# Optimization experiments

Hardware: AMD Instinct MI355X
Metric: run time of the kernel (lower is better)

Reference implementation:

```python
import jax, jax.numpy as jnp
import numpy as np

EPS = 1e-9


def _squash(s, axis=-1):
    # squash(s) = (|s|^2 / (1+|s|^2)) * s / |s|
    sq = jnp.sum(jnp.square(s), axis=axis, keepdims=True)
    norm = jnp.sqrt(sq + EPS)
    return (sq / (1.0 + sq)) * (s / norm)


def setup_inputs() -> dict:
    key = jax.random.key(0)
    B, N_IN, N_OUT, ATOMS = 32, 2048, 64, 16
    votes = jax.random.normal(key, (B, N_IN, N_OUT, ATOMS), dtype=jnp.float32)
    return {"votes": votes, "num_routing": 3}


def reference(votes, num_routing):
    # votes: [B, in_caps, out_caps, atoms]
    temper = 1.0
    softmax_in = False
    B, n_in, n_out, atoms = votes.shape
    logits = jnp.zeros((B, n_in, n_out, 1), dtype=votes.dtype)
    pose = None
    for i in range(num_routing):
        # coupling coefficients: softmax over out-caps axis (softmax_in=False)
        ax = 1 if softmax_in else 2
        c = jax.nn.softmax(logits * temper, axis=ax)  # [B, in, out, 1]
        # weighted pooling over input capsules -> [B, 1, out, atoms]
        preact = jnp.sum(c * votes, axis=1, keepdims=True)
        pose = _squash(preact, axis=-1)
        if i < num_routing - 1:
            # agreement: <votes, pose> over atoms -> [B, in, out, 1]
            logits = logits + jnp.sum(votes * pose, axis=-1, keepdims=True)
    prob = jnp.sqrt(jnp.sum(jnp.square(pose), axis=-1, keepdims=True) + EPS)  # [B,1,out,1]
    pose_out = jnp.squeeze(pose, axis=-3)          # [B, out, atoms]
    prob_out = jnp.squeeze(prob, axis=(-3, -1))    # [B, out]
    return pose_out, prob_out
```

## Files before the change

kernel.cpp:

```cpp
#include <hip/hip_runtime.h>


#define NB 32
#define NIN 2048
#define NOUT 64
#define ATOMS 16
#define EPSF 1e-9f

#define ROWS_PER_WAVE 8
#define WAVES_PER_BLOCK 4
#define ROWS_PER_BLOCK (ROWS_PER_WAVE * WAVES_PER_BLOCK)
#define CHUNKS (NIN / ROWS_PER_BLOCK)
#define RBATCH 4

template <int USE_POSE>
__global__ __launch_bounds__(256, 4) void route_pass(
    const float* __restrict__ votes,
    const float* __restrict__ pose_accum,
    float* __restrict__ preact)
{
    const int b     = blockIdx.x / CHUNKS;
    const int chunk = blockIdx.x % CHUNKS;
    const int wave  = threadIdx.x >> 6;
    const int lane  = threadIdx.x & 63;

    float pose[ATOMS];
    if (USE_POSE) {
        const float4* p4 = reinterpret_cast<const float4*>(pose_accum) + (b * NOUT + lane) * 4;
        float4 q0 = p4[0], q1 = p4[1], q2 = p4[2], q3 = p4[3];
        pose[0]=q0.x; pose[1]=q0.y; pose[2]=q0.z; pose[3]=q0.w;
        pose[4]=q1.x; pose[5]=q1.y; pose[6]=q1.z; pose[7]=q1.w;
        pose[8]=q2.x; pose[9]=q2.y; pose[10]=q2.z; pose[11]=q2.w;
        pose[12]=q3.x; pose[13]=q3.y; pose[14]=q3.z; pose[15]=q3.w;
    }

    float acc[ATOMS];
#pragma unroll
    for (int a = 0; a < ATOMS; ++a) acc[a] = 0.0f;

    const int in0 = chunk * ROWS_PER_BLOCK + wave * ROWS_PER_WAVE;
    const float4* vrow = reinterpret_cast<const float4*>(votes)
                       + ((size_t)(b * NIN + in0) * NOUT + lane) * (ATOMS / 4);

    for (int r0 = 0; r0 < ROWS_PER_WAVE; r0 += RBATCH) {
        float4 c[RBATCH][4];
#pragma unroll
        for (int r = 0; r < RBATCH; ++r) {
            const float4* vp = vrow + (size_t)(r0 + r) * (NOUT * (ATOMS / 4));
            c[r][0] = vp[0]; c[r][1] = vp[1]; c[r][2] = vp[2]; c[r][3] = vp[3];
        }

        float cc[RBATCH];
        if (USE_POSE) {
            float s[RBATCH], e[RBATCH];
#pragma unroll
            for (int r = 0; r < RBATCH; ++r) {
                const float* v = reinterpret_cast<const float*>(&c[r][0]);
                float logit = 0.0f;
#pragma unroll
                for (int a = 0; a < ATOMS; ++a) logit = fmaf(v[a], pose[a], logit);
                e[r] = __expf(logit);
                s[r] = e[r];
            }
#pragma unroll
            for (int mask = 32; mask >= 1; mask >>= 1) {
#pragma unroll
                for (int r = 0; r < RBATCH; ++r)
                    s[r] += __shfl_xor(s[r], mask, 64);
            }
#pragma unroll
            for (int r = 0; r < RBATCH; ++r) cc[r] = e[r] / s[r];
        } else {
#pragma unroll
            for (int r = 0; r < RBATCH; ++r) cc[r] = 1.0f / 64.0f;
        }
#pragma unroll
        for (int r = 0; r < RBATCH; ++r) {
            const float* v = reinterpret_cast<const float*>(&c[r][0]);
#pragma unroll
            for (int a = 0; a < ATOMS; ++a) acc[a] = fmaf(cc[r], v[a], acc[a]);
        }
    }

    __shared__ float red[WAVES_PER_BLOCK * NOUT * ATOMS];
#pragma unroll
    for (int a = 0; a < ATOMS; ++a)
        red[(wave * NOUT + lane) * ATOMS + a] = acc[a];
    __syncthreads();

    for (int idx = threadIdx.x; idx < NOUT * ATOMS; idx += 256) {
        float t = red[idx] + red[NOUT * ATOMS + idx]
                + red[2 * NOUT * ATOMS + idx] + red[3 * NOUT * ATOMS + idx];
        atomicAdd(&preact[b * NOUT * ATOMS + idx], t);
    }
}

__global__ __launch_bounds__(256) void squash_k(
    const float* __restrict__ preact_in,
    float* __restrict__ preact_clr,
    float* __restrict__ pose_accum,
    float* __restrict__ d_out,
    int mode)
{
    int idx = blockIdx.x * 256 + threadIdx.x;
    float s = preact_in[idx];
    float sq = s * s;
#pragma unroll
    for (int mask = 1; mask < ATOMS; mask <<= 1)
        sq += __shfl_xor(sq, mask, 64);
    float norm = sqrtf(sq + EPSF);
    float f = (sq / (1.0f + sq)) / norm;
    float p = f * s;
    if (mode == 0) {
        pose_accum[idx] = p;
        preact_clr[idx] = 0.0f;
    } else if (mode == 1) {
        pose_accum[idx] += p;
        preact_clr[idx] = 0.0f;
    } else {
        d_out[idx] = p;
        if ((idx & (ATOMS - 1)) == 0) {
            float psq = f * f * sq;
            d_out[NB * NOUT * ATOMS + (idx >> 4)] = sqrtf(psq + EPSF);
        }
    }
}

extern "C" void kernel_launch(void* const* d_in, const int* in_sizes, int n_in,
                              void* d_out, int out_size, void* d_ws, size_t ws_size,
                              hipStream_t stream) {
    const float* votes = (const float*)d_in[0];
    float* out = (float*)d_out;

    float* preact     = (float*)d_ws;
    float* pose_accum = preact + NB * NOUT * ATOMS;
    const size_t pre_bytes = (size_t)NB * NOUT * ATOMS * sizeof(float);

    dim3 blk(256);
    dim3 grid_route(NB * CHUNKS);
    dim3 grid_sq(NB * NOUT * ATOMS / 256);

    hipMemsetAsync(preact, 0, pre_bytes, stream);

    route_pass<0><<<grid_route, blk, 0, stream>>>(votes, nullptr, preact);
    squash_k<<<grid_sq, blk, 0, stream>>>(preact, preact, pose_accum, nullptr, 0);

    route_pass<1><<<grid_route, blk, 0, stream>>>(votes, pose_accum, preact);
    squash_k<<<grid_sq, blk, 0, stream>>>(preact, preact, pose_accum, nullptr, 1);

    route_pass<1><<<grid_route, blk, 0, stream>>>(votes, pose_accum, preact);
    squash_k<<<grid_sq, blk, 0, stream>>>(preact, nullptr, nullptr, out, 2);
}
```

Measured before the change: 458.3 us.

## Cache votes as bf16 in first pass and replace atomics with partial-sum reduction

The first routing pass now also writes a bf16 copy of the votes tensor, and the later passes read that half-size copy instead of the fp32 original. This cuts global memory traffic in the two bandwidth-bound agreement passes. Per-block atomicAdd into preact is replaced by per-chunk partial sums that the squash kernel reduces, which also removes the memset. The cost is an extra bf16 write in pass 0, a larger workspace, and reduced precision in the later routing iterations.

```diff
diff --git a/kernel.cpp b/kernel.cpp
--- a/kernel.cpp
+++ b/kernel.cpp
@@ -13,19 +13,82 @@
 #define CHUNKS (NIN / ROWS_PER_BLOCK)
 #define RBATCH 4
 
-template <int USE_POSE>
-__global__ __launch_bounds__(256, 4) void route_pass(
+__device__ __forceinline__ unsigned pack2_bf16(float lo, float hi) {
+    unsigned ul = __float_as_uint(lo);
+    unsigned uh = __float_as_uint(hi);
+    ul = (ul + 0x7fffu + ((ul >> 16) & 1u)) >> 16;
+    uh = (uh + 0x7fffu + ((uh >> 16) & 1u)) & 0xffff0000u;
+    return ul | uh;
+}
+
+__global__ __launch_bounds__(256, 4) void route_pass0(
     const float* __restrict__ votes,
-    const float* __restrict__ pose_accum,
-    float* __restrict__ preact)
+    uint4* __restrict__ votes_bf16,
+    float* __restrict__ partials)
 {
     const int b     = blockIdx.x / CHUNKS;
     const int chunk = blockIdx.x % CHUNKS;
     const int wave  = threadIdx.x >> 6;
     const int lane  = threadIdx.x & 63;
 
+    float acc[ATOMS];
+#pragma unroll
+    for (int a = 0; a < ATOMS; ++a) acc[a] = 0.0f;
+
+    const int in0 = chunk * ROWS_PER_BLOCK + wave * ROWS_PER_WAVE;
+    const float4* vrow = reinterpret_cast<const float4*>(votes)
+                       + ((size_t)(b * NIN + in0) * NOUT + lane) * 4;
+    uint4* brow = votes_bf16 + ((size_t)(b * NIN + in0) * NOUT + lane) * 2;
+
+    for (int r0 = 0; r0 < ROWS_PER_WAVE; r0 += RBATCH) {
+        float4 c[RBATCH][4];
+#pragma unroll
+        for (int r = 0; r < RBATCH; ++r) {
+            const float4* vp = vrow + (size_t)(r0 + r) * (NOUT * 4);
+            c[r][0] = vp[0]; c[r][1] = vp[1]; c[r][2] = vp[2]; c[r][3] = vp[3];
+        }
+#pragma unroll
+        for (int r = 0; r < RBATCH; ++r) {
+            const float* v = reinterpret_cast<const float*>(&c[r][0]);
+#pragma unroll
+            for (int a = 0; a < ATOMS; ++a) acc[a] += v[a];
+            uint4 p0, p1;
+            p0.x = pack2_bf16(v[0],  v[1]);  p0.y = pack2_bf16(v[2],  v[3]);
+            p0.z = pack2_bf16(v[4],  v[5]);  p0.w = pack2_bf16(v[6],  v[7]);
+            p1.x = pack2_bf16(v[8],  v[9]);  p1.y = pack2_bf16(v[10], v[11]);
+            p1.z = pack2_bf16(v[12], v[13]); p1.w = pack2_bf16(v[14], v[15]);
+            uint4* bp = brow + (size_t)(r0 + r) * (NOUT * 2);
+            bp[0] = p0; bp[1] = p1;
+        }
+    }
+#pragma unroll
+    for (int a = 0; a < ATOMS; ++a) acc[a] *= (1.0f / 64.0f);
+
+    __shared__ float red[WAVES_PER_BLOCK * NOUT * ATOMS];
+#pragma unroll
+    for (int a = 0; a < ATOMS; ++a)
+        red[(wave * NOUT + lane) * ATOMS + a] = acc[a];
+    __syncthreads();
+
+    float* pblock = partials + ((size_t)(b * CHUNKS + chunk) << 10);
+    for (int idx = threadIdx.x; idx < NOUT * ATOMS; idx += 256) {
+        pblock[idx] = red[idx] + red[NOUT * ATOMS + idx]
+                    + red[2 * NOUT * ATOMS + idx] + red[3 * NOUT * ATOMS + idx];
+    }
+}
+
+__global__ __launch_bounds__(256, 4) void route_passN(
+    const uint4* __restrict__ votes_bf16,
+    const float* __restrict__ pose_accum,
+    float* __restrict__ partials)
+{
+    const int b     = blockIdx.x / CHUNKS;
+    const int chunk = blockIdx.x % CHUNKS;
+    const int wave  = threadIdx.x >> 6;
+    const int lane  = threadIdx.x & 63;
+
     float pose[ATOMS];
-    if (USE_POSE) {
+    {
         const float4* p4 = reinterpret_cast<const float4*>(pose_accum) + (b * NOUT + lane) * 4;
         float4 q0 = p4[0], q1 = p4[1], q2 = p4[2], q3 = p4[3];
         pose[0]=q0.x; pose[1]=q0.y; pose[2]=q0.z; pose[3]=q0.w;
@@ -39,46 +102,45 @@
     for (int a = 0; a < ATOMS; ++a) acc[a] = 0.0f;
 
     const int in0 = chunk * ROWS_PER_BLOCK + wave * ROWS_PER_WAVE;
-    const float4* vrow = reinterpret_cast<const float4*>(votes)
-                       + ((size_t)(b * NIN + in0) * NOUT + lane) * (ATOMS / 4);
+    const uint4* brow = votes_bf16 + ((size_t)(b * NIN + in0) * NOUT + lane) * 2;
 
     for (int r0 = 0; r0 < ROWS_PER_WAVE; r0 += RBATCH) {
-        float4 c[RBATCH][4];
-#pragma unroll
-        for (int r = 0; r < RBATCH; ++r) {
-            const float4* vp = vrow + (size_t)(r0 + r) * (NOUT * (ATOMS / 4));
-            c[r][0] = vp[0]; c[r][1] = vp[1]; c[r][2] = vp[2]; c[r][3] = vp[3];
-        }
-
-        float cc[RBATCH];
-        if (USE_POSE) {
-            float s[RBATCH], e[RBATCH];
-#pragma unroll
-            for (int r = 0; r < RBATCH; ++r) {
-                const float* v = reinterpret_cast<const float*>(&c[r][0]);
-                float logit = 0.0f;
-#pragma unroll
-                for (int a = 0; a < ATOMS; ++a) logit = fmaf(v[a], pose[a], logit);
-                e[r] = __expf(logit);
-                s[r] = e[r];
+        uint4 raw[RBATCH][2];
+#pragma unroll
+        for (int r = 0; r < RBATCH; ++r) {
+            const uint4* bp = brow + (size_t)(r0 + r) * (NOUT * 2);
+            raw[r][0] = bp[0]; raw[r][1] = bp[1];
+        }
+        float v[RBATCH][ATOMS];
+#pragma unroll
+        for (int r = 0; r < RBATCH; ++r) {
+            const unsigned* u = reinterpret_cast<const unsigned*>(&raw[r][0]);
+#pragma unroll
+            for (int k = 0; k < 8; ++k) {
+                v[r][2*k]   = __uint_as_float(u[k] << 16);
+                v[r][2*k+1] = __uint_as_float(u[k] & 0xffff0000u);
             }
-#pragma unroll
-            for (int mask = 32; mask >= 1; mask >>= 1) {
-#pragma unroll
-                for (int r = 0; r < RBATCH; ++r)
-                    s[r] += __shfl_xor(s[r], mask, 64);
-            }
-#pragma unroll
-            for (int r = 0; r < RBATCH; ++r) cc[r] = e[r] / s[r];
-        } else {
-#pragma unroll
-            for (int r = 0; r < RBATCH; ++r) cc[r] = 1.0f / 64.0f;
-        }
-#pragma unroll
-        for (int r = 0; r < RBATCH; ++r) {
-            const float* v = reinterpret_cast<const float*>(&c[r][0]);
-#pragma unroll
-            for (int a = 0; a < ATOMS; ++a) acc[a] = fmaf(cc[r], v[a], acc[a]);
+        }
+        float e[RBATCH], s[RBATCH];
+#pragma unroll
+        for (int r = 0; r < RBATCH; ++r) {
+            float logit = 0.0f;
+#pragma unroll
+            for (int a = 0; a < ATOMS; ++a) logit = fmaf(v[r][a], pose[a], logit);
+            e[r] = __expf(logit);
+            s[r] = e[r];
+        }
+#pragma unroll
+        for (int mask = 32; mask >= 1; mask >>= 1) {
+#pragma unroll
+            for (int r = 0; r < RBATCH; ++r)
+                s[r] += __shfl_xor(s[r], mask, 64);
+        }
+#pragma unroll
+        for (int r = 0; r < RBATCH; ++r) {
+            float cc = e[r] / s[r];
+#pragma unroll
+            for (int a = 0; a < ATOMS; ++a) acc[a] = fmaf(cc, v[r][a], acc[a]);
         }
     }
 
@@ -88,40 +150,49 @@
         red[(wave * NOUT + lane) * ATOMS + a] = acc[a];
     __syncthreads();
 
+    float* pblock = partials + ((size_t)(b * CHUNKS + chunk) << 10);
     for (int idx = threadIdx.x; idx < NOUT * ATOMS; idx += 256) {
-        float t = red[idx] + red[NOUT * ATOMS + idx]
-                + red[2 * NOUT * ATOMS + idx] + red[3 * NOUT * ATOMS + idx];
-        atomicAdd(&preact[b * NOUT * ATOMS + idx], t);
-    }
-}
-
-__global__ __launch_bounds__(256) void squash_k(
-    const float* __restrict__ preact_in,
-    float* __restrict__ preact_clr,
+        pblock[idx] = red[idx] + red[NOUT * ATOMS + idx]
+                    + red[2 * NOUT * ATOMS + idx] + red[3 * NOUT * ATOMS + idx];
+    }
+}
+
+__global__ __launch_bounds__(256) void squash_reduce(
+    const float* __restrict__ partials,
     float* __restrict__ pose_accum,
     float* __restrict__ d_out,
     int mode)
 {
-    int idx = blockIdx.x * 256 + threadIdx.x;
-    float s = preact_in[idx];
+    int gid = blockIdx.x * 256 + threadIdx.x;
+    int b  = gid >> 10;
+    int oa = gid & 1023;
+    const float* p = partials + ((size_t)b << 16) + oa;
+    float s0 = 0.0f, s1 = 0.0f, s2 = 0.0f, s3 = 0.0f;
+#pragma unroll
+    for (int c = 0; c < CHUNKS; c += 4) {
+        s0 += p[(c + 0) << 10];
+        s1 += p[(c + 1) << 10];
+        s2 += p[(c + 2) << 10];
+        s3 += p[(c + 3) << 10];
+    }
+    float s = (s0 + s1) + (s2 + s3);
+
     float sq = s * s;
 #pragma unroll
     for (int mask = 1; mask < ATOMS; mask <<= 1)
         sq += __shfl_xor(sq, mask, 64);
     float norm = sqrtf(sq + EPSF);
     float f = (sq / (1.0f + sq)) / norm;
-    float p = f * s;
+    float pse = f * s;
     if (mode == 0) {
-        pose_accum[idx] = p;
-        preact_clr[idx] = 0.0f;
+        pose_accum[gid] = pse;
     } else if (mode == 1) {
-        pose_accum[idx] += p;
-        preact_clr[idx] = 0.0f;
+        pose_accum[gid] += pse;
     } else {
-        d_out[idx] = p;
-        if ((idx & (ATOMS - 1)) == 0) {
+        d_out[gid] = pse;
+        if ((gid & (ATOMS - 1)) == 0) {
             float psq = f * f * sq;
-            d_out[NB * NOUT * ATOMS + (idx >> 4)] = sqrtf(psq + EPSF);
+            d_out[NB * NOUT * ATOMS + (gid >> 4)] = sqrtf(psq + EPSF);
         }
     }
 }
@@ -132,22 +203,20 @@
     const float* votes = (const float*)d_in[0];
     float* out = (float*)d_out;
 
-    float* preact     = (float*)d_ws;
-    float* pose_accum = preact + NB * NOUT * ATOMS;
-    const size_t pre_bytes = (size_t)NB * NOUT * ATOMS * sizeof(float);
+    float* pose_accum = (float*)d_ws;
+    float* partials   = pose_accum + NB * NOUT * ATOMS;
+    uint4* votes_bf16 = (uint4*)(partials + (size_t)NB * CHUNKS * NOUT * ATOMS);
 
     dim3 blk(256);
     dim3 grid_route(NB * CHUNKS);
     dim3 grid_sq(NB * NOUT * ATOMS / 256);
 
-    hipMemsetAsync(preact, 0, pre_bytes, stream);
-
-    route_pass<0><<<grid_route, blk, 0, stream>>>(votes, nullptr, preact);
-    squash_k<<<grid_sq, blk, 0, stream>>>(preact, preact, pose_accum, nullptr, 0);
-
-    route_pass<1><<<grid_route, blk, 0, stream>>>(votes, pose_accum, preact);
-    squash_k<<<grid_sq, blk, 0, stream>>>(preact, preact, pose_accum, nullptr, 1);
-
-    route_pass<1><<<grid_route, blk, 0, stream>>>(votes, pose_accum, preact);
-    squash_k<<<grid_sq, blk, 0, stream>>>(preact, nullptr, nullptr, out, 2);
-}
+    route_pass0<<<grid_route, blk, 0, stream>>>(votes, votes_bf16, partials);
+    squash_reduce<<<grid_sq, blk, 0, stream>>>(partials, pose_accum, nullptr, 0);
+
+    route_passN<<<grid_route, blk, 0, stream>>>(votes_bf16, pose_accum, partials);
+    squash_reduce<<<grid_sq, blk, 0, stream>>>(partials, pose_accum, nullptr, 1);
+
+    route_passN<<<grid_route, blk, 0, stream>>>(votes_bf16, pose_accum, partials);
+    squash_reduce<<<grid_sq, blk, 0, stream>>>(partials, nullptr, out, 2);
+}
```

Result: slower. 526.3 us (+14.8%).

## Coalesce vote loads across lanes and replace atomics with partial-sum reduction

Applied to the files above, without the earlier changes.

Each lane now reads a contiguous float4, so a wave covers consecutive memory instead of each lane striding through its own 64-byte row. This needs partial dot products combined across 4 lanes with shuffles before the softmax. Float atomicAdd into preact is replaced by per-block partial buffers that squash_reduce sums over all chunks, which also removes the memset. The cost is extra workspace traffic (about 8MB of partials per pass) and a larger reduction in the squash kernel.

```diff
diff --git a/kernel.cpp b/kernel.cpp
--- a/kernel.cpp
+++ b/kernel.cpp
@@ -11,117 +11,161 @@
 #define WAVES_PER_BLOCK 4
 #define ROWS_PER_BLOCK (ROWS_PER_WAVE * WAVES_PER_BLOCK)
 #define CHUNKS (NIN / ROWS_PER_BLOCK)
-#define RBATCH 4
+#define RBATCH 2
 
 template <int USE_POSE>
 __global__ __launch_bounds__(256, 4) void route_pass(
-    const float* __restrict__ votes,
-    const float* __restrict__ pose_accum,
-    float* __restrict__ preact)
+    const float4* __restrict__ votes4,
+    const float4* __restrict__ pose_accum4,
+    float4* __restrict__ partials4)
 {
     const int b     = blockIdx.x / CHUNKS;
     const int chunk = blockIdx.x % CHUNKS;
     const int wave  = threadIdx.x >> 6;
     const int lane  = threadIdx.x & 63;
 
-    float pose[ATOMS];
+    float4 pse[4];
     if (USE_POSE) {
-        const float4* p4 = reinterpret_cast<const float4*>(pose_accum) + (b * NOUT + lane) * 4;
-        float4 q0 = p4[0], q1 = p4[1], q2 = p4[2], q3 = p4[3];
-        pose[0]=q0.x; pose[1]=q0.y; pose[2]=q0.z; pose[3]=q0.w;
-        pose[4]=q1.x; pose[5]=q1.y; pose[6]=q1.z; pose[7]=q1.w;
-        pose[8]=q2.x; pose[9]=q2.y; pose[10]=q2.z; pose[11]=q2.w;
-        pose[12]=q3.x; pose[13]=q3.y; pose[14]=q3.z; pose[15]=q3.w;
+#pragma unroll
+        for (int j = 0; j < 4; ++j)
+            pse[j] = pose_accum4[(b * NOUT + j * 16 + (lane >> 2)) * 4 + (lane & 3)];
     }
 
-    float acc[ATOMS];
+    float4 acc[4];
 #pragma unroll
-    for (int a = 0; a < ATOMS; ++a) acc[a] = 0.0f;
+    for (int j = 0; j < 4; ++j) acc[j] = make_float4(0.f, 0.f, 0.f, 0.f);
 
     const int in0 = chunk * ROWS_PER_BLOCK + wave * ROWS_PER_WAVE;
-    const float4* vrow = reinterpret_cast<const float4*>(votes)
-                       + ((size_t)(b * NIN + in0) * NOUT + lane) * (ATOMS / 4);
+    const float4* vrow = votes4 + (size_t)(b * NIN + in0) * 256 + lane;
 
     for (int r0 = 0; r0 < ROWS_PER_WAVE; r0 += RBATCH) {
-        float4 c[RBATCH][4];
+        float4 v[RBATCH][4];
 #pragma unroll
         for (int r = 0; r < RBATCH; ++r) {
-            const float4* vp = vrow + (size_t)(r0 + r) * (NOUT * (ATOMS / 4));
-            c[r][0] = vp[0]; c[r][1] = vp[1]; c[r][2] = vp[2]; c[r][3] = vp[3];
+            const float4* vp = vrow + (size_t)(r0 + r) * 256;
+#pragma unroll
+            for (int j = 0; j < 4; ++j) v[r][j] = vp[j * 64];
         }
 
-        float cc[RBATCH];
         if (USE_POSE) {
-            float s[RBATCH], e[RBATCH];
+            float lg[RBATCH][4];
+#pragma unroll
+            for (int r = 0; r < RBATCH; ++r)
+#pragma unroll
+                for (int j = 0; j < 4; ++j) {
+                    float d = v[r][j].x * pse[j].x;
+                    d = fmaf(v[r][j].y, pse[j].y, d);
+                    d = fmaf(v[r][j].z, pse[j].z, d);
+                    d = fmaf(v[r][j].w, pse[j].w, d);
+                    lg[r][j] = d;
+                }
+#pragma unroll
+            for (int mask = 1; mask <= 2; mask <<= 1)
+#pragma unroll
+                for (int r = 0; r < RBATCH; ++r)
+#pragma unroll
+                    for (int j = 0; j < 4; ++j)
+                        lg[r][j] += __shfl_xor(lg[r][j], mask, 64);
+
+            float e[RBATCH][4], s[RBATCH];
 #pragma unroll
             for (int r = 0; r < RBATCH; ++r) {
-                const float* v = reinterpret_cast<const float*>(&c[r][0]);
-                float logit = 0.0f;
+                float t = 0.f;
 #pragma unroll
-                for (int a = 0; a < ATOMS; ++a) logit = fmaf(v[a], pose[a], logit);
-                e[r] = __expf(logit);
-                s[r] = e[r];
+                for (int j = 0; j < 4; ++j) { e[r][j] = __expf(lg[r][j]); t += e[r][j]; }
+                s[r] = t;
             }
 #pragma unroll
-            for (int mask = 32; mask >= 1; mask >>= 1) {
+            for (int mask = 4; mask <= 32; mask <<= 1)
 #pragma unroll
                 for (int r = 0; r < RBATCH; ++r)
                     s[r] += __shfl_xor(s[r], mask, 64);
+
+#pragma unroll
+            for (int r = 0; r < RBATCH; ++r) {
+                float inv = __frcp_rn(s[r]);
+#pragma unroll
+                for (int j = 0; j < 4; ++j) {
+                    float c = e[r][j] * inv;
+                    acc[j].x = fmaf(c, v[r][j].x, acc[j].x);
+                    acc[j].y = fmaf(c, v[r][j].y, acc[j].y);
+                    acc[j].z = fmaf(c, v[r][j].z, acc[j].z);
+                    acc[j].w = fmaf(c, v[r][j].w, acc[j].w);
+                }
             }
-#pragma unroll
-            for (int r = 0; r < RBATCH; ++r) cc[r] = e[r] / s[r];
         } else {
 #pragma unroll
-            for (int r = 0; r < RBATCH; ++r) cc[r] = 1.0f / 64.0f;
+            for (int r = 0; r < RBATCH; ++r)
+#pragma unroll
+                for (int j = 0; j < 4; ++j) {
+                    acc[j].x += v[r][j].x; acc[j].y += v[r][j].y;
+                    acc[j].z += v[r][j].z; acc[j].w += v[r][j].w;
+                }
         }
+    }
+    if (!USE_POSE) {
 #pragma unroll
-        for (int r = 0; r < RBATCH; ++r) {
-            const float* v = reinterpret_cast<const float*>(&c[r][0]);
-#pragma unroll
-            for (int a = 0; a < ATOMS; ++a) acc[a] = fmaf(cc[r], v[a], acc[a]);
+        for (int j = 0; j < 4; ++j) {
+            acc[j].x *= (1.f / 64.f); acc[j].y *= (1.f / 64.f);
+            acc[j].z *= (1.f / 64.f); acc[j].w *= (1.f / 64.f);
         }
     }
 
-    __shared__ float red[WAVES_PER_BLOCK * NOUT * ATOMS];
+    __shared__ float4 red4[WAVES_PER_BLOCK * 256];
 #pragma unroll
-    for (int a = 0; a < ATOMS; ++a)
-        red[(wave * NOUT + lane) * ATOMS + a] = acc[a];
+    for (int j = 0; j < 4; ++j)
+        red4[wave * 256 + j * 64 + lane] = acc[j];
     __syncthreads();
 
-    for (int idx = threadIdx.x; idx < NOUT * ATOMS; idx += 256) {
-        float t = red[idx] + red[NOUT * ATOMS + idx]
-                + red[2 * NOUT * ATOMS + idx] + red[3 * NOUT * ATOMS + idx];
-        atomicAdd(&preact[b * NOUT * ATOMS + idx], t);
+    float4* pblock4 = partials4 + ((size_t)(b * CHUNKS + chunk) << 8);
+    {
+        int idx = threadIdx.x;
+        float4 a = red4[idx], b2 = red4[256 + idx], c = red4[512 + idx], d = red4[768 + idx];
+        float4 t;
+        t.x = (a.x + b2.x) + (c.x + d.x);
+        t.y = (a.y + b2.y) + (c.y + d.y);
+        t.z = (a.z + b2.z) + (c.z + d.z);
+        t.w = (a.w + b2.w) + (c.w + d.w);
+        pblock4[idx] = t;
     }
 }
 
-__global__ __launch_bounds__(256) void squash_k(
-    const float* __restrict__ preact_in,
-    float* __restrict__ preact_clr,
+__global__ __launch_bounds__(256) void squash_reduce(
+    const float* __restrict__ partials,
     float* __restrict__ pose_accum,
     float* __restrict__ d_out,
     int mode)
 {
-    int idx = blockIdx.x * 256 + threadIdx.x;
-    float s = preact_in[idx];
+    int gid = blockIdx.x * 256 + threadIdx.x;
+    int b  = gid >> 10;
+    int oa = gid & 1023;
+    const float* p = partials + ((size_t)b << 16) + oa;
+    float s0 = 0.f, s1 = 0.f, s2 = 0.f, s3 = 0.f;
+#pragma unroll
+    for (int c = 0; c < CHUNKS; c += 4) {
+        s0 += p[(c + 0) << 10];
+        s1 += p[(c + 1) << 10];
+        s2 += p[(c + 2) << 10];
+        s3 += p[(c + 3) << 10];
+    }
+    float s = (s0 + s1) + (s2 + s3);
+
     float sq = s * s;
 #pragma unroll
     for (int mask = 1; mask < ATOMS; mask <<= 1)
         sq += __shfl_xor(sq, mask, 64);
     float norm = sqrtf(sq + EPSF);
     float f = (sq / (1.0f + sq)) / norm;
-    float p = f * s;
+    float pse = f * s;
     if (mode == 0) {
-        pose_accum[idx] = p;
-        preact_clr[idx] = 0.0f;
+        pose_accum[gid] = pse;
     } else if (mode == 1) {
-        pose_accum[idx] += p;
-        preact_clr[idx] = 0.0f;
+        pose_accum[gid] += pse;
     } else {
-        d_out[idx] = p;
-        if ((idx & (ATOMS - 1)) == 0) {
+        d_out[gid] = pse;
+        if ((gid & (ATOMS - 1)) == 0) {
             float psq = f * f * sq;
-            d_out[NB * NOUT * ATOMS + (idx >> 4)] = sqrtf(psq + EPSF);
+            d_out[NB * NOUT * ATOMS + (gid >> 4)] = sqrtf(psq + EPSF);
         }
     }
 }
@@ -129,25 +173,22 @@
 extern "C" void kernel_launch(void* const* d_in, const int* in_sizes, int n_in,
                               void* d_out, int out_size, void* d_ws, size_t ws_size,
                               hipStream_t stream) {
-    const float* votes = (const float*)d_in[0];
+    const float4* votes4 = (const float4*)d_in[0];
     float* out = (float*)d_out;
 
-    float* preact     = (float*)d_ws;
-    float* pose_accum = preact + NB * NOUT * ATOMS;
-    const size_t pre_bytes = (size_t)NB * NOUT * ATOMS * sizeof(float);
+    float* pose_accum = (float*)d_ws;
+    float* partials   = pose_accum + NB * NOUT * ATOMS;
 
     dim3 blk(256);
     dim3 grid_route(NB * CHUNKS);
     dim3 grid_sq(NB * NOUT * ATOMS / 256);
 
-    hipMemsetAsync(preact, 0, pre_bytes, stream);
+    route_pass<0><<<grid_route, blk, 0, stream>>>(votes4, nullptr, (float4*)partials);
+    squash_reduce<<<grid_sq, blk, 0, stream>>>(partials, pose_accum, nullptr, 0);
 
-    route_pass<0><<<grid_route, blk, 0, stream>>>(votes, nullptr, preact);
-    squash_k<<<grid_sq, blk, 0, stream>>>(preact, preact, pose_accum, nullptr, 0);
+    route_pass<1><<<grid_route, blk, 0, stream>>>(votes4, (const float4*)pose_accum, (float4*)partials);
+    squash_reduce<<<grid_sq, blk, 0, stream>>>(partials, pose_accum, nullptr, 1);
 
-    route_pass<1><<<grid_route, blk, 0, stream>>>(votes, pose_accum, preact);
-    squash_k<<<grid_sq, blk, 0, stream>>>(preact, preact, pose_accum, nullptr, 1);
-
-    route_pass<1><<<grid_route, blk, 0, stream>>>(votes, pose_accum, preact);
-    squash_k<<<grid_sq, blk, 0, stream>>>(preact, nullptr, nullptr, out, 2);
+    route_pass<1><<<grid_route, blk, 0, stream>>>(votes4, (const float4*)pose_accum, (float4*)partials);
+    squash_reduce<<<grid_sq, blk, 0, stream>>>(partials, nullptr, out, 2);
 }
```

Result: faster. 446.4 us (-2.6%).
